# Performance work log

Hardware: AMD Instinct MI355X
Metric: run time of the kernel (lower is better)

## Reference

```python
import jax, jax.numpy as jnp
import numpy as np


def setup_inputs() -> dict:
    key = jax.random.key(0)
    k1, k2, k3, k4 = jax.random.split(key, 4)
    B, S, I, O = 2, 4096, 4096, 4096
    x = jax.random.normal(k1, (B, S, I), dtype=jnp.float32)
    # packed int4 weights: each byte holds two nibbles; [O, I//2]
    qweight = jax.random.randint(k2, (O, I // 2), 0, 256, dtype=jnp.int32)
    # per-tensor weight scale (scalar, stored as shape [1])
    weight_scale = jax.random.uniform(k3, (1,), dtype=jnp.float32) * 0.01 + 1e-3
    bias = jax.random.normal(k4, (O,), dtype=jnp.float32)
    return {"x": x, "qweight": qweight, "weight_scale": weight_scale, "bias": bias}


def _dequant_weight(qweight, weight_scale):
    # unpack_int4 (dim=1): high nibble -> even cols, low nibble -> odd cols
    high = (qweight >> 4) - 8           # [O, I//2], values in [-8, 7]
    low = (qweight & 15) - 8            # [O, I//2]
    unpacked = jnp.stack([high, low], axis=-1).reshape(qweight.shape[0], -1)  # [O, I]
    # no weight_offset -> w = q * scale
    return unpacked.astype(weight_scale.dtype) * weight_scale


def reference(x, qweight, weight_scale, bias):
    w = _dequant_weight(qweight, weight_scale)  # [O, I] fp32
    # dynamic per-tensor symmetric int8 activation quantization
    max_abs = jnp.max(jnp.abs(x))
    scale = max_abs / 127.0
    scale = jnp.where(scale == 0, jnp.ones_like(scale), scale)
    x_dq = jnp.round(x / scale) * scale  # fake-quantized activations (offset = 0)
    # F.linear: x @ w.T + bias
    out = jnp.einsum('bsi,oi->bso', x_dq, w) + bias
    return out.astype(x.dtype)
```

## Files before the change

### kernel.cpp

```cpp
#include <hip/hip_runtime.h>


typedef __attribute__((ext_vector_type(4))) int int32x4;

__device__ __forceinline__ void async_copy16(const void* gsrc, void* ldsdst) {
  __builtin_amdgcn_global_load_lds(
      (const __attribute__((address_space(1))) void*)gsrc,
      (__attribute__((address_space(3))) void*)ldsdst, 16, 0, 0);
}

__global__ void amax_kernel(const float* __restrict__ x,
                            float* __restrict__ partial, int n4) {
  int tid = blockIdx.x * blockDim.x + threadIdx.x;
  int stride = gridDim.x * blockDim.x;
  float m = 0.0f;
  const float4* x4 = (const float4*)x;
  for (int i = tid; i < n4; i += stride) {
    float4 v = x4[i];
    m = fmaxf(m, fmaxf(fmaxf(fabsf(v.x), fabsf(v.y)),
                       fmaxf(fabsf(v.z), fabsf(v.w))));
  }
#pragma unroll
  for (int off = 32; off > 0; off >>= 1)
    m = fmaxf(m, __shfl_down(m, off, 64));
  __shared__ float red[4];
  if ((threadIdx.x & 63) == 0) red[threadIdx.x >> 6] = m;
  __syncthreads();
  if (threadIdx.x == 0) {
    partial[blockIdx.x] = fmaxf(fmaxf(red[0], red[1]), fmaxf(red[2], red[3]));
  }
}

__global__ void amax_reduce(const float* __restrict__ partial,
                            float* __restrict__ amax) {
  const int t = threadIdx.x;
  float m = fmaxf(partial[t], partial[t + 256]);
#pragma unroll
  for (int off = 32; off > 0; off >>= 1)
    m = fmaxf(m, __shfl_down(m, off, 64));
  __shared__ float red[4];
  if ((t & 63) == 0) red[t >> 6] = m;
  __syncthreads();
  if (t == 0)
    *amax = fmaxf(fmaxf(red[0], red[1]), fmaxf(red[2], red[3]));
}

__global__ void quant_kernel(const float* __restrict__ x,
                             const float* __restrict__ amax_p,
                             unsigned* __restrict__ qx, int n4) {
  float s = *amax_p / 127.0f;
  if (s == 0.0f) s = 1.0f;
  const float inv = 1.0f / s;
  int tid = blockIdx.x * blockDim.x + threadIdx.x;
  int stride = gridDim.x * blockDim.x;
  const float4* x4 = (const float4*)x;
  for (int i = tid; i < n4; i += stride) {
    float4 v = x4[i];
    int a = __float2int_rn(v.x * inv);
    int b = __float2int_rn(v.y * inv);
    int c = __float2int_rn(v.z * inv);
    int d = __float2int_rn(v.w * inv);
    qx[i] = (unsigned)(a & 0xFF) | ((unsigned)(b & 0xFF) << 8) |
            ((unsigned)(c & 0xFF) << 16) | ((unsigned)(d & 0xFF) << 24);
  }
}

__device__ __forceinline__ unsigned pack2(int q) {
  unsigned hi = (unsigned)((((q >> 4) & 15) - 8) & 0xFF);
  unsigned lo = (unsigned)(((q & 15) - 8) & 0xFF);
  return hi | (lo << 8);
}

__global__ void repack_kernel(const int* __restrict__ qw,
                              uint2* __restrict__ w8, int n4) {
  int tid = blockIdx.x * blockDim.x + threadIdx.x;
  int stride = gridDim.x * blockDim.x;
  const int4* q4 = (const int4*)qw;
  for (int i = tid; i < n4; i += stride) {
    int4 q = q4[i];
    uint2 r;
    r.x = pack2(q.x) | (pack2(q.y) << 16);
    r.y = pack2(q.z) | (pack2(q.w) << 16);
    w8[i] = r;
  }
}

#define BM 256
#define BN 256
#define BKT 64
#define TILE_B (BM * BKT)

__global__ __launch_bounds__(512, 2) void gemm_i8(
    const char* __restrict__ A, const char* __restrict__ Bt,
    const float* __restrict__ bias, const float* __restrict__ amax_p,
    const float* __restrict__ wscale, float* __restrict__ C,
    int M, int N, int K) {
  __shared__ alignas(16) char As[4 * TILE_B];
  __shared__ alignas(16) char Bs[4 * TILE_B];

  const int tid = threadIdx.x;
  const int lane = tid & 63;
  const int wave = tid >> 6;
  const int wm = wave >> 2;
  const int wn = wave & 3;
  const int quad = lane >> 4;
  const int l16 = lane & 15;

  const int cpx = gridDim.x >> 3;
  const int wg = (blockIdx.x & 7) * cpx + (blockIdx.x >> 3);
  const int bM = (wg >> 4) * BM;
  const int bN = (wg & 15) * BN;

  const int NT = K >> 6;

  const int srow = tid >> 2;
  const int scoff = (((tid & 3) ^ ((tid >> 3) & 3)) << 4);
  const char* aS = A + (size_t)(bM + srow) * K + scoff;
  const char* bS = Bt + (size_t)(bN + srow) * K + scoff;
  const size_t skip = (size_t)128 * K;
  char* aD = &As[tid * 16];
  char* bD = &Bs[tid * 16];

  for (int tt = 0; tt < 3; ++tt) {
    const int boff = tt * TILE_B;
    const char* sa = aS + tt * BKT;
    const char* sb = bS + tt * BKT;
    async_copy16(sa, aD + boff);
    async_copy16(sa + skip, aD + boff + 8192);
    async_copy16(sb, bD + boff);
    async_copy16(sb + skip, bD + boff + 8192);
  }

  const int xsl = ((quad ^ ((l16 >> 1) & 3)) << 4);
  const int arow0 = (wm << 7) + l16;
  const int brow0 = (wn << 6) + l16;

  int32x4 acc[8][4] = {};

  for (int t = 0; t < NT; ++t) {
    if (t + 2 < NT)
      asm volatile("s_waitcnt vmcnt(8)" ::: "memory");
    else if (t + 1 < NT)
      asm volatile("s_waitcnt vmcnt(4)" ::: "memory");
    else
      asm volatile("s_waitcnt vmcnt(0)" ::: "memory");
    __builtin_amdgcn_s_barrier();
    __builtin_amdgcn_sched_barrier(0);

    const char* Ab = &As[(t & 3) * TILE_B];
    const char* Bb = &Bs[(t & 3) * TILE_B];
    const int pboff = ((t + 3) & 3) * TILE_B;
    const bool do_stage = (t + 3 < NT);

    int32x4 af[4], bf[4];

#pragma unroll
    for (int i = 0; i < 4; ++i)
      af[i] = *(const int32x4*)(Ab + (arow0 + i * 16) * BKT + xsl);
#pragma unroll
    for (int j = 0; j < 4; ++j)
      bf[j] = *(const int32x4*)(Bb + (brow0 + j * 16) * BKT + xsl);
    if (do_stage) {
      const char* sa = aS + (t + 3) * BKT;
      async_copy16(sa, aD + pboff);
      async_copy16(sa + skip, aD + pboff + 8192);
    }
    __builtin_amdgcn_s_barrier();
    __builtin_amdgcn_s_setprio(1);
#pragma unroll
    for (int i = 0; i < 4; ++i)
#pragma unroll
      for (int j = 0; j < 4; ++j)
        acc[i][j] = __builtin_amdgcn_mfma_i32_16x16x64_i8(af[i], bf[j],
                                                          acc[i][j], 0, 0, 0);
    __builtin_amdgcn_s_setprio(0);

#pragma unroll
    for (int i = 0; i < 4; ++i)
      af[i] = *(const int32x4*)(Ab + (arow0 + 64 + i * 16) * BKT + xsl);
    if (do_stage) {
      const char* sb = bS + (t + 3) * BKT;
      async_copy16(sb, bD + pboff);
      async_copy16(sb + skip, bD + pboff + 8192);
    }
    __builtin_amdgcn_s_barrier();
    __builtin_amdgcn_s_setprio(1);
#pragma unroll
    for (int i = 0; i < 4; ++i)
#pragma unroll
      for (int j = 0; j < 4; ++j)
        acc[4 + i][j] = __builtin_amdgcn_mfma_i32_16x16x64_i8(
            af[i], bf[j], acc[4 + i][j], 0, 0, 0);
    __builtin_amdgcn_s_setprio(0);
  }

  float s = *amax_p / 127.0f;
  if (s == 0.0f) s = 1.0f;
  const float cs = s * wscale[0];

#pragma unroll
  for (int f = 0; f < 8; ++f) {
#pragma unroll
    for (int j = 0; j < 4; ++j) {
      const int n = bN + (wn << 6) + j * 16 + l16;
#pragma unroll
      for (int r = 0; r < 4; ++r) {
        const int m = bM + (wm << 7) + f * 16 + quad * 4 + r;
        C[(size_t)m * N + n] = (float)acc[f][j][r] * cs + bias[n];
      }
    }
  }
}

extern "C" void kernel_launch(void* const* d_in, const int* in_sizes, int n_in,
                              void* d_out, int out_size, void* d_ws,
                              size_t ws_size, hipStream_t stream) {
  const float* x = (const float*)d_in[0];
  const int* qw = (const int*)d_in[1];
  const float* wscale = (const float*)d_in[2];
  const float* bias = (const float*)d_in[3];
  float* out = (float*)d_out;

  const int nx = in_sizes[0];
  const int npacked = in_sizes[1];
  const int O = in_sizes[3];
  const int I = (npacked / O) * 2;
  const int M = nx / I;

  float* amax = (float*)d_ws;
  float* partial = (float*)((char*)d_ws + 256);
  char* qx = (char*)d_ws + 8192;
  char* w8 = qx + (size_t)nx;

  amax_kernel<<<512, 256, 0, stream>>>(x, partial, nx / 4);
  amax_reduce<<<1, 256, 0, stream>>>(partial, amax);
  quant_kernel<<<2048, 256, 0, stream>>>(x, amax, (unsigned*)qx, nx / 4);
  repack_kernel<<<1024, 256, 0, stream>>>(qw, (uint2*)w8, npacked / 4);

  const int nwg = (M / BM) * (O / BN);
  gemm_i8<<<nwg, 512, 0, stream>>>(qx, w8, bias, amax, wscale, out, M, O, I);
}
```

Measured before the change: 406.9 us.

## Software-pipeline LDS fragment loads across k-tiles and fuse amax reduce into quant

Restructures the int8 GEMM main loop into a two-tile unrolled macro with double-buffered register fragments. The next tile's A/B fragments are loaded from LDS while the second half of the current tile's MFMAs is still to run, and each iteration now has one barrier instead of two. Separately, the single-block amax reduction is folded into the quant kernel: every block re-reduces the 512 partials, and block 0 writes the result, which removes one kernel launch. The risks are higher register pressure from the extra fragment buffers and redundant partial reads in every quant block.

After: 397.1 us. 2.4% less time.

```diff
diff --git a/kernel.cpp b/kernel.cpp
--- a/kernel.cpp
+++ b/kernel.cpp
@@ -31,8 +31,10 @@
   }
 }
 
-__global__ void amax_reduce(const float* __restrict__ partial,
-                            float* __restrict__ amax) {
+__global__ void quant_kernel(const float* __restrict__ x,
+                             const float* __restrict__ partial,
+                             float* __restrict__ amax_out,
+                             unsigned* __restrict__ qx, int n4) {
   const int t = threadIdx.x;
   float m = fmaxf(partial[t], partial[t + 256]);
 #pragma unroll
@@ -41,17 +43,18 @@
   __shared__ float red[4];
   if ((t & 63) == 0) red[t >> 6] = m;
   __syncthreads();
-  if (t == 0)
-    *amax = fmaxf(fmaxf(red[0], red[1]), fmaxf(red[2], red[3]));
-}
-
-__global__ void quant_kernel(const float* __restrict__ x,
-                             const float* __restrict__ amax_p,
-                             unsigned* __restrict__ qx, int n4) {
-  float s = *amax_p / 127.0f;
-  if (s == 0.0f) s = 1.0f;
-  const float inv = 1.0f / s;
-  int tid = blockIdx.x * blockDim.x + threadIdx.x;
+  __shared__ float s_bcast;
+  if (t == 0) {
+    float amax = fmaxf(fmaxf(red[0], red[1]), fmaxf(red[2], red[3]));
+    if (blockIdx.x == 0) *amax_out = amax;
+    float s = amax / 127.0f;
+    if (s == 0.0f) s = 1.0f;
+    s_bcast = 1.0f / s;
+  }
+  __syncthreads();
+  const float inv = s_bcast;
+
+  int tid = blockIdx.x * blockDim.x + t;
   int stride = gridDim.x * blockDim.x;
   const float4* x4 = (const float4*)x;
   for (int i = tid; i < n4; i += stride) {
@@ -90,6 +93,60 @@
 #define BKT 64
 #define TILE_B (BM * BKT)
 
+#define TILE_BODY(t, CUR_AL, CUR_BF, NXT_AL, NXT_BF)                          \
+  {                                                                           \
+    const char* Ab = &As[((t) & 3) * TILE_B];                                 \
+     \
+    _Pragma("unroll") for (int i = 0; i < 4; ++i) afH[i] =                    \
+        *(const int32x4*)(Ab + (arow0 + 64 + i * 16) * BKT + xsl);            \
+    if ((t) + 3 < NT) {                                                       \
+      const char* sa = aS + ((t) + 3) * BKT;                                  \
+      char* ad = aD + (((t) + 3) & 3) * TILE_B;                               \
+      async_copy16(sa, ad);                                                   \
+      async_copy16(sa + skip, ad + 8192);                                     \
+    }                                                                         \
+     \
+    asm volatile("s_waitcnt lgkmcnt(4)" ::: "memory");                        \
+    __builtin_amdgcn_s_setprio(1);                                            \
+    _Pragma("unroll") for (int i = 0; i < 4; ++i)                             \
+        _Pragma("unroll") for (int j = 0; j < 4; ++j) acc[i][j] =             \
+            __builtin_amdgcn_mfma_i32_16x16x64_i8(CUR_AL[i], CUR_BF[j],       \
+                                                  acc[i][j], 0, 0, 0);        \
+    __builtin_amdgcn_s_setprio(0);                                            \
+           \
+    if ((t) + 1 < NT) {                                                       \
+           \
+      asm volatile("s_waitcnt lgkmcnt(0)" ::: "memory");                      \
+        \
+      if ((t) + 4 <= NT)                                                      \
+        asm volatile("s_waitcnt vmcnt(6)" ::: "memory");                      \
+      else if ((t) + 3 <= NT)                                                 \
+        asm volatile("s_waitcnt vmcnt(4)" ::: "memory");                      \
+      else                                                                    \
+        asm volatile("s_waitcnt vmcnt(0)" ::: "memory");                      \
+      __builtin_amdgcn_s_barrier();                                           \
+      __builtin_amdgcn_sched_barrier(0);    \
+      const char* Abn = &As[(((t) + 1) & 3) * TILE_B];                        \
+      const char* Bbn = &Bs[(((t) + 1) & 3) * TILE_B];                        \
+      _Pragma("unroll") for (int i = 0; i < 4; ++i) NXT_AL[i] =               \
+          *(const int32x4*)(Abn + (arow0 + i * 16) * BKT + xsl);              \
+      _Pragma("unroll") for (int j = 0; j < 4; ++j) NXT_BF[j] =               \
+          *(const int32x4*)(Bbn + (brow0 + j * 16) * BKT + xsl);              \
+    }                                                                         \
+    if ((t) + 3 < NT) {                                                       \
+      const char* sb = bS + ((t) + 3) * BKT;                                  \
+      char* bd = bD + (((t) + 3) & 3) * TILE_B;                               \
+      async_copy16(sb, bd);                                                   \
+      async_copy16(sb + skip, bd + 8192);                                     \
+    }                                                                         \
+    __builtin_amdgcn_s_setprio(1);                                            \
+    _Pragma("unroll") for (int i = 0; i < 4; ++i)                             \
+        _Pragma("unroll") for (int j = 0; j < 4; ++j) acc[4 + i][j] =         \
+            __builtin_amdgcn_mfma_i32_16x16x64_i8(afH[i], CUR_BF[j],          \
+                                                  acc[4 + i][j], 0, 0, 0);    \
+    __builtin_amdgcn_s_setprio(0);                                            \
+  }
+
 __global__ __launch_bounds__(512, 2) void gemm_i8(
     const char* __restrict__ A, const char* __restrict__ Bt,
     const float* __restrict__ bias, const float* __restrict__ amax_p,
@@ -136,62 +193,22 @@
   const int brow0 = (wn << 6) + l16;
 
   int32x4 acc[8][4] = {};
-
-  for (int t = 0; t < NT; ++t) {
-    if (t + 2 < NT)
-      asm volatile("s_waitcnt vmcnt(8)" ::: "memory");
-    else if (t + 1 < NT)
-      asm volatile("s_waitcnt vmcnt(4)" ::: "memory");
-    else
-      asm volatile("s_waitcnt vmcnt(0)" ::: "memory");
-    __builtin_amdgcn_s_barrier();
-    __builtin_amdgcn_sched_barrier(0);
-
-    const char* Ab = &As[(t & 3) * TILE_B];
-    const char* Bb = &Bs[(t & 3) * TILE_B];
-    const int pboff = ((t + 3) & 3) * TILE_B;
-    const bool do_stage = (t + 3 < NT);
-
-    int32x4 af[4], bf[4];
-
-#pragma unroll
-    for (int i = 0; i < 4; ++i)
-      af[i] = *(const int32x4*)(Ab + (arow0 + i * 16) * BKT + xsl);
-#pragma unroll
-    for (int j = 0; j < 4; ++j)
-      bf[j] = *(const int32x4*)(Bb + (brow0 + j * 16) * BKT + xsl);
-    if (do_stage) {
-      const char* sa = aS + (t + 3) * BKT;
-      async_copy16(sa, aD + pboff);
-      async_copy16(sa + skip, aD + pboff + 8192);
-    }
-    __builtin_amdgcn_s_barrier();
-    __builtin_amdgcn_s_setprio(1);
-#pragma unroll
-    for (int i = 0; i < 4; ++i)
-#pragma unroll
-      for (int j = 0; j < 4; ++j)
-        acc[i][j] = __builtin_amdgcn_mfma_i32_16x16x64_i8(af[i], bf[j],
-                                                          acc[i][j], 0, 0, 0);
-    __builtin_amdgcn_s_setprio(0);
-
-#pragma unroll
-    for (int i = 0; i < 4; ++i)
-      af[i] = *(const int32x4*)(Ab + (arow0 + 64 + i * 16) * BKT + xsl);
-    if (do_stage) {
-      const char* sb = bS + (t + 3) * BKT;
-      async_copy16(sb, bD + pboff);
-      async_copy16(sb + skip, bD + pboff + 8192);
-    }
-    __builtin_amdgcn_s_barrier();
-    __builtin_amdgcn_s_setprio(1);
-#pragma unroll
-    for (int i = 0; i < 4; ++i)
-#pragma unroll
-      for (int j = 0; j < 4; ++j)
-        acc[4 + i][j] = __builtin_amdgcn_mfma_i32_16x16x64_i8(
-            af[i], bf[j], acc[4 + i][j], 0, 0, 0);
-    __builtin_amdgcn_s_setprio(0);
+  int32x4 afL0[4], bf0[4], afL1[4], bf1[4], afH[4];
+
+  asm volatile("s_waitcnt vmcnt(8)" ::: "memory");
+  __builtin_amdgcn_s_barrier();
+  __builtin_amdgcn_sched_barrier(0);
+
+#pragma unroll
+  for (int i = 0; i < 4; ++i)
+    afL0[i] = *(const int32x4*)(&As[0] + (arow0 + i * 16) * BKT + xsl);
+#pragma unroll
+  for (int j = 0; j < 4; ++j)
+    bf0[j] = *(const int32x4*)(&Bs[0] + (brow0 + j * 16) * BKT + xsl);
+
+  for (int t = 0; t < NT; t += 2) {
+    TILE_BODY(t, afL0, bf0, afL1, bf1);
+    TILE_BODY(t + 1, afL1, bf1, afL0, bf0);
   }
 
   float s = *amax_p / 127.0f;
@@ -233,8 +250,8 @@
   char* w8 = qx + (size_t)nx;
 
   amax_kernel<<<512, 256, 0, stream>>>(x, partial, nx / 4);
-  amax_reduce<<<1, 256, 0, stream>>>(partial, amax);
-  quant_kernel<<<2048, 256, 0, stream>>>(x, amax, (unsigned*)qx, nx / 4);
+  quant_kernel<<<2048, 256, 0, stream>>>(x, partial, amax, (unsigned*)qx,
+                                         nx / 4);
   repack_kernel<<<1024, 256, 0, stream>>>(qw, (uint2*)w8, npacked / 4);
 
   const int nwg = (M / BM) * (O / BN);
```
